# Kernel tuning notes

Measured on AMD Instinct MI355X. Metric: run time of the kernel, lower is better.

## Reference

```python
import jax, jax.numpy as jnp
import numpy as np

N_NODES = 100000
N_EDGES = 3200000
N_GRAPHS = 1000
C = 11   # atomic features
D = 4    # bond features
BN_EPS = 1e-5


def setup_inputs() -> dict:
    key = jax.random.key(0)
    ks = jax.random.split(key, 20)
    inp = {
        "x": jax.random.normal(ks[0], (N_NODES, C), dtype=jnp.float32),
        "edge_index": jax.random.randint(ks[1], (2, N_EDGES), 0, N_NODES),
        "edge_attr": jax.random.uniform(ks[2], (N_EDGES, D), dtype=jnp.float32),
        "batch": jnp.sort(jax.random.randint(ks[3], (N_NODES,), 0, N_GRAPHS)),
    }
    s = 0.3
    # CGConv layer 1 params: lin_f, lin_s take z=[x_i, x_j, e] of dim 2C+D
    inp["Wf1"] = jax.random.normal(ks[4], (2 * C + D, C), dtype=jnp.float32) * s
    inp["bf1"] = jnp.zeros((C,), jnp.float32)
    inp["Ws1"] = jax.random.normal(ks[5], (2 * C + D, C), dtype=jnp.float32) * s
    inp["bs1"] = jnp.zeros((C,), jnp.float32)
    inp["gamma1"] = jnp.ones((C,), jnp.float32)
    inp["beta1"] = jnp.zeros((C,), jnp.float32)
    # CGConv layer 2
    inp["Wf2"] = jax.random.normal(ks[6], (2 * C + D, C), dtype=jnp.float32) * s
    inp["bf2"] = jnp.zeros((C,), jnp.float32)
    inp["Ws2"] = jax.random.normal(ks[7], (2 * C + D, C), dtype=jnp.float32) * s
    inp["bs2"] = jnp.zeros((C,), jnp.float32)
    inp["gamma2"] = jnp.ones((C,), jnp.float32)
    inp["beta2"] = jnp.zeros((C,), jnp.float32)
    # MLP head
    inp["W_fc1"] = jax.random.normal(ks[8], (C, 5), dtype=jnp.float32) * s
    inp["b_fc1"] = jnp.zeros((5,), jnp.float32)
    inp["W_fc2"] = jax.random.normal(ks[9], (5, 1), dtype=jnp.float32) * s
    inp["b_fc2"] = jnp.zeros((1,), jnp.float32)
    return inp


def _cgconv(x, src, dst, e, Wf, bf, Ws, bs, gamma, beta):
    # z = [x_i, x_j, e_ij] per edge; message = sigmoid(lin_f(z)) * softplus(lin_s(z))
    z = jnp.concatenate([x[dst], x[src], e], axis=-1)          # [E, 2C+D]
    msg = jax.nn.sigmoid(z @ Wf + bf) * jax.nn.softplus(z @ Ws + bs)  # [E, C]
    agg = jax.ops.segment_sum(msg, dst, num_segments=N_NODES)  # [N, C]
    # BatchNorm1d (training-mode: batch statistics over nodes)
    mu = jnp.mean(agg, axis=0)
    var = jnp.var(agg, axis=0)
    agg = (agg - mu) * jax.lax.rsqrt(var + BN_EPS) * gamma + beta
    return x + agg  # residual


def reference(x, edge_index, edge_attr, batch,
              Wf1, bf1, Ws1, bs1, gamma1, beta1,
              Wf2, bf2, Ws2, bs2, gamma2, beta2,
              W_fc1, b_fc1, W_fc2, b_fc2):
    src, dst = edge_index[0], edge_index[1]
    h = _cgconv(x, src, dst, edge_attr, Wf1, bf1, Ws1, bs1, gamma1, beta1)
    h = _cgconv(h, src, dst, edge_attr, Wf2, bf2, Ws2, bs2, gamma2, beta2)
    # global mean pool per graph
    sums = jax.ops.segment_sum(h, batch, num_segments=N_GRAPHS)        # [G, C]
    cnts = jax.ops.segment_sum(jnp.ones((h.shape[0],), h.dtype), batch,
                               num_segments=N_GRAPHS)
    pooled = sums / jnp.maximum(cnts, 1.0)[:, None]
    out = jax.nn.softplus(pooled @ W_fc1 + b_fc1)
    out = out @ W_fc2 + b_fc2                                          # [G, 1]
    return out
```

## Files before the change

kernel.cpp:

```cpp
#include <hip/hip_runtime.h>
#include <hip/hip_fp16.h>
#include <math.h>

#define N_NODES 100000
#define N_EDGES 3200000
#define N_GRAPHS 1000
#define C 11
#define D 4
#define AST 12
#define XWST 24
#define XHST 16
#define BN_EPS 1e-5f
#define LOG2E 1.44269504088896f
#define LN2   0.69314718055994f
#define QSCALE (1.0f/65535.0f)

#define BSHIFT 8
#define BNODES 256
#define NB ((N_NODES + BNODES - 1) / BNODES)
#define SUBS 8
#define CAP2 1280
#define EPB 8192
#define PBLK ((N_EDGES + EPB - 1) / EPB)
#define SB 64
#define PST 48

__device__ __forceinline__ float fast_sigmoid(float x) {
    float e = exp2f(-LOG2E * x);
    return __builtin_amdgcn_rcpf(1.0f + e);
}
__device__ __forceinline__ float fast_softplus(float x) {
    float e = exp2f(LOG2E * x);
    float l = log2f(1.0f + e) * LN2;
    return (x > 20.0f) ? x : l;
}
__device__ __forceinline__ unsigned packh2(float a, float b) {
    __half2 h = __floats2half2_rn(a, b);
    return *reinterpret_cast<unsigned*>(&h);
}
__device__ __forceinline__ float2 unpackh2(unsigned u) {
    __half2 h = *reinterpret_cast<__half2*>(&u);
    return __half22float2(h);
}

__global__ void __launch_bounds__(1024) partition_kernel(
    const int* __restrict__ ei, const float4* __restrict__ ea,
    int* __restrict__ bcur2, uint3* __restrict__ grp)
{
    __shared__ int lh[NB];
    __shared__ int lbase[NB];
    for (int i = threadIdx.x; i < NB; i += 1024) lh[i] = 0;
    __syncthreads();
    int sub = blockIdx.x & (SUBS - 1);
    int e0 = blockIdx.x * EPB;
    for (int r = 0; r < EPB; r += 1024) {
        int e = e0 + r + threadIdx.x;
        if (e < N_EDGES) atomicAdd(&lh[ei[N_EDGES + e] >> BSHIFT], 1);
    }
    __syncthreads();
    for (int b = threadIdx.x; b < NB; b += 1024) {
        lbase[b] = atomicAdd(&bcur2[b * SUBS + sub], lh[b]);
        lh[b] = 0;
    }
    __syncthreads();
    for (int r = 0; r < EPB; r += 1024) {
        int e = e0 + r + threadIdx.x;
        if (e < N_EDGES) {
            int d = ei[N_EDGES + e];
            int s = ei[e];
            float4 v = ea[e];
            unsigned q0 = (unsigned)(v.x * 65535.0f + 0.5f);
            unsigned q1 = (unsigned)(v.y * 65535.0f + 0.5f);
            unsigned q2 = (unsigned)(v.z * 65535.0f + 0.5f);
            unsigned q3 = (unsigned)(v.w * 65535.0f + 0.5f);
            int b = d >> BSHIFT;
            int ofs = lbase[b] + atomicAdd(&lh[b], 1);
            if (ofs < CAP2)
                grp[((size_t)b * SUBS + sub) * CAP2 + ofs] =
                    make_uint3((unsigned)s | ((unsigned)(d & 255) << 17),
                               q0 | (q1 << 16), q2 | (q3 << 16));
        }
    }
}

__global__ void __launch_bounds__(512) bscan_kernel(
    const int* __restrict__ bcur2, int* __restrict__ bexcl, int* __restrict__ off)
{
    __shared__ int wsum[8];
    int t = threadIdx.x;
    int lane = t & 63, w = t >> 6;
    int v = 0;
    if (t < NB) {
        #pragma unroll
        for (int s = 0; s < SUBS; ++s) v += min(bcur2[t * SUBS + s], CAP2);
    }
    int incl = v;
    #pragma unroll
    for (int d = 1; d < 64; d <<= 1) {
        int u = __shfl_up(incl, d);
        if (lane >= d) incl += u;
    }
    if (lane == 63) wsum[w] = incl;
    __syncthreads();
    if (w == 0) {
        int x = (lane < 8) ? wsum[lane] : 0;
        #pragma unroll
        for (int d = 1; d < 8; d <<= 1) {
            int u = __shfl_up(x, d);
            if (lane >= d) x += u;
        }
        if (lane < 8) wsum[lane] = x;
    }
    __syncthreads();
    int excl = incl - v + (w > 0 ? wsum[w - 1] : 0);
    if (t < NB) bexcl[t] = excl;
    if (t == NB - 1) off[N_NODES] = excl + v;
}

__global__ void __launch_bounds__(512) finalize_kernel(
    const uint3* __restrict__ grp, const int* __restrict__ bcur2,
    const int* __restrict__ bexcl,
    int* __restrict__ off, uint3* __restrict__ rec)
{
    __shared__ int lcnt[BNODES];
    __shared__ int lexcl[BNODES];
    __shared__ int wsum[4];
    int b = blockIdx.x;
    int base = bexcl[b];
    int t = threadIdx.x;
    if (t < BNODES) lcnt[t] = 0;
    __syncthreads();
    for (int s = 0; s < SUBS; ++s) {
        int cs = min(bcur2[b * SUBS + s], CAP2);
        const uint3* g = grp + ((size_t)b * SUBS + s) * CAP2;
        for (int i = t; i < cs; i += 512)
            atomicAdd(&lcnt[(g[i].x >> 17) & 255], 1);
    }
    __syncthreads();
    if (t < BNODES) {
        int lane = t & 63, w = t >> 6;
        int v = lcnt[t];
        int incl = v;
        #pragma unroll
        for (int d = 1; d < 64; d <<= 1) {
            int u = __shfl_up(incl, d);
            if (lane >= d) incl += u;
        }
        if (lane == 63) wsum[w] = incl;
        __syncthreads();
        if (w == 0) {
            int x = (lane < 4) ? wsum[lane] : 0;
            #pragma unroll
            for (int d = 1; d < 4; d <<= 1) {
                int u = __shfl_up(x, d);
                if (lane >= d) x += u;
            }
            if (lane < 4) wsum[lane] = x;
        }
        __syncthreads();
        int excl = incl - v + (w > 0 ? wsum[w - 1] : 0);
        lexcl[t] = excl;
        int n = (b << BSHIFT) + t;
        if (n < N_NODES) off[n] = base + excl;
        lcnt[t] = 0;
    } else {
        __syncthreads();
        __syncthreads();
    }
    __syncthreads();
    for (int s = 0; s < SUBS; ++s) {
        int cs = min(bcur2[b * SUBS + s], CAP2);
        const uint3* g = grp + ((size_t)b * SUBS + s) * CAP2;
        for (int i = t; i < cs; i += 512) {
            uint3 r = g[i];
            int nl = (r.x >> 17) & 255;
            int pos = base + lexcl[nl] + atomicAdd(&lcnt[nl], 1);
            rec[pos] = make_uint3(r.x & 0x1FFFFu, r.y, r.z);
        }
    }
}

__global__ void __launch_bounds__(256) pre_kernel(
    const float* __restrict__ xin, int stride,
    const float* __restrict__ Wf, const float* __restrict__ Ws,
    const float* __restrict__ bf, const float* __restrict__ bs,
    float* __restrict__ xwd, unsigned* __restrict__ xwsh)
{
    __shared__ float sW[22 * C * 2];
    __shared__ float sbf[C], sbs[C];
    for (int i = threadIdx.x; i < 22 * C; i += blockDim.x) {
        sW[2 * i] = Wf[i];
        sW[2 * i + 1] = Ws[i];
    }
    if (threadIdx.x < C) { sbf[threadIdx.x] = bf[threadIdx.x]; sbs[threadIdx.x] = bs[threadIdx.x]; }
    __syncthreads();

    int n = blockIdx.x * blockDim.x + threadIdx.x;
    if (n >= N_NODES) return;
    float xi[C];
    #pragma unroll
    for (int j = 0; j < C; ++j) xi[j] = xin[n * stride + j];

    float od[XWST];
    unsigned oh[12];
    #pragma unroll
    for (int c = 0; c < C; ++c) {
        float f = sbf[c], s = sbs[c];
        float f2 = 0.0f, s2 = 0.0f;
        #pragma unroll
        for (int j = 0; j < C; ++j) {
            f  = fmaf(xi[j], sW[2 * (j * C + c)], f);
            s  = fmaf(xi[j], sW[2 * (j * C + c) + 1], s);
            f2 = fmaf(xi[j], sW[2 * ((C + j) * C + c)], f2);
            s2 = fmaf(xi[j], sW[2 * ((C + j) * C + c) + 1], s2);
        }
        od[2 * c] = f; od[2 * c + 1] = s;
        oh[c] = packh2(f2, s2);
    }
    od[22] = 0.0f; od[23] = 0.0f; oh[11] = 0u;
    float4* pd = (float4*)(xwd + (size_t)n * XWST);
    #pragma unroll
    for (int i = 0; i < 6; ++i)
        pd[i] = make_float4(od[4 * i], od[4 * i + 1], od[4 * i + 2], od[4 * i + 3]);
    uint4* ph = (uint4*)(xwsh + (size_t)n * XHST);
    #pragma unroll
    for (int i = 0; i < 3; ++i)
        ph[i] = make_uint4(oh[4 * i], oh[4 * i + 1], oh[4 * i + 2], oh[4 * i + 3]);
}

__global__ void __launch_bounds__(256) conv_kernel(
    const uint3* __restrict__ rec, const int* __restrict__ off,
    const float* __restrict__ xwd, const unsigned* __restrict__ xwsh,
    const float* __restrict__ Wf, const float* __restrict__ Ws,
    float* __restrict__ agg)
{
    int tid = blockIdx.x * blockDim.x + threadIdx.x;
    int n = tid >> 3;
    int t = tid & 7;
    if (n >= N_NODES) return;

    float weaf[44], weas[44];
    {
        const float2* pf = (const float2*)(Wf + 22 * C);
        const float2* ps = (const float2*)(Ws + 22 * C);
        #pragma unroll
        for (int i = 0; i < 22; ++i) {
            float2 a = pf[i], b = ps[i];
            weaf[2 * i] = a.x; weaf[2 * i + 1] = a.y;
            weas[2 * i] = b.x; weas[2 * i + 1] = b.y;
        }
    }
    float based[XWST];
    {
        const float4* pd = (const float4*)(xwd + (size_t)n * XWST);
        #pragma unroll
        for (int i = 0; i < 6; ++i) {
            float4 a = pd[i];
            based[4 * i] = a.x; based[4 * i + 1] = a.y;
            based[4 * i + 2] = a.z; based[4 * i + 3] = a.w;
        }
    }

    float acc[C];
    #pragma unroll
    for (int c = 0; c < C; ++c) acc[c] = 0.0f;

    int e1 = off[n + 1];
    for (int k = off[n] + t; k < e1; k += 8) {
        uint3 r = rec[k];
        int src = (int)r.x;
        float ea0 = (float)(r.y & 0xFFFFu) * QSCALE;
        float ea1 = (float)(r.y >> 16) * QSCALE;
        float ea2 = (float)(r.z & 0xFFFFu) * QSCALE;
        float ea3 = (float)(r.z >> 16) * QSCALE;
        const uint4* px = (const uint4*)(xwsh + (size_t)src * XHST);
        uint4 ha = px[0], hb = px[1], hc = px[2];
        float2 xv[C];
        xv[0] = unpackh2(ha.x); xv[1] = unpackh2(ha.y);
        xv[2] = unpackh2(ha.z); xv[3] = unpackh2(ha.w);
        xv[4] = unpackh2(hb.x); xv[5] = unpackh2(hb.y);
        xv[6] = unpackh2(hb.z); xv[7] = unpackh2(hb.w);
        xv[8] = unpackh2(hc.x); xv[9] = unpackh2(hc.y);
        xv[10] = unpackh2(hc.z);
        #pragma unroll
        for (int c = 0; c < C; ++c) {
            float f = based[2 * c] + xv[c].x;
            float s = based[2 * c + 1] + xv[c].y;
            f = fmaf(ea0, weaf[c], f);         s = fmaf(ea0, weas[c], s);
            f = fmaf(ea1, weaf[C + c], f);     s = fmaf(ea1, weas[C + c], s);
            f = fmaf(ea2, weaf[2 * C + c], f); s = fmaf(ea2, weas[2 * C + c], s);
            f = fmaf(ea3, weaf[3 * C + c], f); s = fmaf(ea3, weas[3 * C + c], s);
            acc[c] += fast_sigmoid(f) * fast_softplus(s);
        }
    }

    #pragma unroll
    for (int c = 0; c < C; ++c) {
        acc[c] += __shfl_xor(acc[c], 1);
        acc[c] += __shfl_xor(acc[c], 2);
        acc[c] += __shfl_xor(acc[c], 4);
    }
    if (t == 0) {
        float4* pa = (float4*)(agg + (size_t)n * AST);
        pa[0] = make_float4(acc[0], acc[1], acc[2], acc[3]);
        pa[1] = make_float4(acc[4], acc[5], acc[6], acc[7]);
        pa[2] = make_float4(acc[8], acc[9], acc[10], 0.0f);
    }
}

__global__ void __launch_bounds__(256) bn_stats_kernel(
    const float* __restrict__ agg, float* __restrict__ pstats)
{
    float s[C], q[C];
    #pragma unroll
    for (int c = 0; c < C; ++c) { s[c] = 0.0f; q[c] = 0.0f; }
    for (int n = blockIdx.x * 256 + threadIdx.x; n < N_NODES; n += SB * 256) {
        const float4* pa = (const float4*)(agg + (size_t)n * AST);
        float4 a0 = pa[0], a1 = pa[1], a2 = pa[2];
        float v[C] = {a0.x, a0.y, a0.z, a0.w, a1.x, a1.y, a1.z, a1.w,
                      a2.x, a2.y, a2.z};
        #pragma unroll
        for (int c = 0; c < C; ++c) { s[c] += v[c]; q[c] += v[c] * v[c]; }
    }
    #pragma unroll
    for (int c = 0; c < C; ++c) {
        #pragma unroll
        for (int o = 32; o > 0; o >>= 1) {
            s[c] += __shfl_down(s[c], o);
            q[c] += __shfl_down(q[c], o);
        }
    }
    __shared__ float ls[2 * C + 2];
    if (threadIdx.x < 2 * C + 2) ls[threadIdx.x] = 0.0f;
    __syncthreads();
    if ((threadIdx.x & 63) == 0) {
        #pragma unroll
        for (int c = 0; c < C; ++c) {
            atomicAdd(&ls[2 * c], s[c]);
            atomicAdd(&ls[2 * c + 1], q[c]);
        }
    }
    __syncthreads();
    if (threadIdx.x < 2 * C)
        pstats[blockIdx.x * PST + threadIdx.x] = ls[threadIdx.x];
}

__device__ __forceinline__ void reduce_stats(
    const float* __restrict__ pstats, float* smu, float* srs)
{
    if (threadIdx.x < C) {
        double sum = 0.0, sq = 0.0;
        for (int b = 0; b < SB; ++b) {
            sum += (double)pstats[b * PST + 2 * threadIdx.x];
            sq  += (double)pstats[b * PST + 2 * threadIdx.x + 1];
        }
        double mu = sum / (double)N_NODES;
        double var = sq / (double)N_NODES - mu * mu;
        smu[threadIdx.x] = (float)mu;
        srs[threadIdx.x] = (float)(1.0 / sqrt(var + (double)BN_EPS));
    }
}

__global__ void __launch_bounds__(256) bnpre_kernel(
    const float* __restrict__ xin, const float* __restrict__ agg,
    const float* __restrict__ pstats,
    const float* __restrict__ gamma, const float* __restrict__ beta,
    const float* __restrict__ Wf, const float* __restrict__ Ws,
    const float* __restrict__ bf, const float* __restrict__ bs,
    float* __restrict__ hout, float* __restrict__ xwd, unsigned* __restrict__ xwsh)
{
    __shared__ float sW[22 * C * 2];
    __shared__ float sbf[C], sbs[C];
    __shared__ float smu[C], srs[C], sg[C], sb[C];
    for (int i = threadIdx.x; i < 22 * C; i += blockDim.x) {
        sW[2 * i] = Wf[i];
        sW[2 * i + 1] = Ws[i];
    }
    reduce_stats(pstats, smu, srs);
    if (threadIdx.x < C) {
        sbf[threadIdx.x] = bf[threadIdx.x];
        sbs[threadIdx.x] = bs[threadIdx.x];
        sg[threadIdx.x] = gamma[threadIdx.x];
        sb[threadIdx.x] = beta[threadIdx.x];
    }
    __syncthreads();

    int n = blockIdx.x * blockDim.x + threadIdx.x;
    if (n >= N_NODES) return;

    float hv[C];
    #pragma unroll
    for (int c = 0; c < C; ++c) {
        float a = agg[n * AST + c];
        hv[c] = xin[n * C + c] + (a - smu[c]) * srs[c] * sg[c] + sb[c];
    }
    {
        float4* ph = (float4*)(hout + (size_t)n * AST);
        ph[0] = make_float4(hv[0], hv[1], hv[2], hv[3]);
        ph[1] = make_float4(hv[4], hv[5], hv[6], hv[7]);
        ph[2] = make_float4(hv[8], hv[9], hv[10], 0.0f);
    }

    float od[XWST];
    unsigned oh[12];
    #pragma unroll
    for (int c = 0; c < C; ++c) {
        float f = sbf[c], s = sbs[c];
        float f2 = 0.0f, s2 = 0.0f;
        #pragma unroll
        for (int j = 0; j < C; ++j) {
            f  = fmaf(hv[j], sW[2 * (j * C + c)], f);
            s  = fmaf(hv[j], sW[2 * (j * C + c) + 1], s);
            f2 = fmaf(hv[j], sW[2 * ((C + j) * C + c)], f2);
            s2 = fmaf(hv[j], sW[2 * ((C + j) * C + c) + 1], s2);
        }
        od[2 * c] = f; od[2 * c + 1] = s;
        oh[c] = packh2(f2, s2);
    }
    od[22] = 0.0f; od[23] = 0.0f; oh[11] = 0u;
    float4* pd = (float4*)(xwd + (size_t)n * XWST);
    #pragma unroll
    for (int i = 0; i < 6; ++i)
        pd[i] = make_float4(od[4 * i], od[4 * i + 1], od[4 * i + 2], od[4 * i + 3]);
    uint4* ph2 = (uint4*)(xwsh + (size_t)n * XHST);
    #pragma unroll
    for (int i = 0; i < 3; ++i)
        ph2[i] = make_uint4(oh[4 * i], oh[4 * i + 1], oh[4 * i + 2], oh[4 * i + 3]);
}

__global__ void __launch_bounds__(256) bn_apply_kernel(
    const float* __restrict__ hin, const float* __restrict__ agg,
    const float* __restrict__ pstats,
    const float* __restrict__ gamma, const float* __restrict__ beta,
    float* __restrict__ hout)
{
    __shared__ float smu[C], srs[C], sg[C], sb[C];
    reduce_stats(pstats, smu, srs);
    if (threadIdx.x < C) {
        sg[threadIdx.x] = gamma[threadIdx.x];
        sb[threadIdx.x] = beta[threadIdx.x];
    }
    __syncthreads();
    int n = blockIdx.x * blockDim.x + threadIdx.x;
    if (n >= N_NODES) return;
    float hv[C];
    #pragma unroll
    for (int c = 0; c < C; ++c) {
        float a = agg[n * AST + c];
        hv[c] = hin[n * AST + c] + (a - smu[c]) * srs[c] * sg[c] + sb[c];
    }
    float4* ph = (float4*)(hout + (size_t)n * AST);
    ph[0] = make_float4(hv[0], hv[1], hv[2], hv[3]);
    ph[1] = make_float4(hv[4], hv[5], hv[6], hv[7]);
    ph[2] = make_float4(hv[8], hv[9], hv[10], 0.0f);
}

__global__ void __launch_bounds__(256) pool_kernel(
    const float* __restrict__ h, const int* __restrict__ batch,
    float* __restrict__ gsum, float* __restrict__ gcnt)
{
    const int PER = 8;
    int t = blockIdx.x * blockDim.x + threadIdx.x;
    int start = t * PER;
    if (start >= N_NODES) return;
    int end = min(start + PER, N_NODES);

    int g = batch[start];
    float acc[C];
    #pragma unroll
    for (int c = 0; c < C; ++c) acc[c] = 0.0f;
    float cnt = 0.0f;
    for (int n = start; n < end; ++n) {
        int gn = batch[n];
        if (gn != g) {
            #pragma unroll
            for (int c = 0; c < C; ++c) atomicAdd(&gsum[g * C + c], acc[c]);
            atomicAdd(&gcnt[g], cnt);
            g = gn;
            #pragma unroll
            for (int c = 0; c < C; ++c) acc[c] = 0.0f;
            cnt = 0.0f;
        }
        #pragma unroll
        for (int c = 0; c < C; ++c) acc[c] += h[n * AST + c];
        cnt += 1.0f;
    }
    #pragma unroll
    for (int c = 0; c < C; ++c) atomicAdd(&gsum[g * C + c], acc[c]);
    atomicAdd(&gcnt[g], cnt);
}

__global__ void __launch_bounds__(256) head_kernel(
    const float* __restrict__ gsum, const float* __restrict__ gcnt,
    const float* __restrict__ W1, const float* __restrict__ b1,
    const float* __restrict__ W2, const float* __restrict__ b2,
    float* __restrict__ out)
{
    int g = blockIdx.x * blockDim.x + threadIdx.x;
    if (g >= N_GRAPHS) return;
    float cnt = fmaxf(gcnt[g], 1.0f);
    float p[C];
    #pragma unroll
    for (int c = 0; c < C; ++c) p[c] = gsum[g * C + c] / cnt;
    float acc = b2[0];
    #pragma unroll
    for (int j = 0; j < 5; ++j) {
        float t = b1[j];
        #pragma unroll
        for (int c = 0; c < C; ++c) t = fmaf(p[c], W1[c * 5 + j], t);
        acc = fmaf(fast_softplus(t), W2[j], acc);
    }
    out[g] = acc;
}

extern "C" void kernel_launch(void* const* d_in, const int* in_sizes, int n_in,
                              void* d_out, int out_size, void* d_ws, size_t ws_size,
                              hipStream_t stream) {
    const float* x   = (const float*)d_in[0];
    const int*   ei  = (const int*)d_in[1];
    const float* ea  = (const float*)d_in[2];
    const int*   bat = (const int*)d_in[3];
    const float* Wf1 = (const float*)d_in[4];
    const float* bf1 = (const float*)d_in[5];
    const float* Ws1 = (const float*)d_in[6];
    const float* bs1 = (const float*)d_in[7];
    const float* g1  = (const float*)d_in[8];
    const float* be1 = (const float*)d_in[9];
    const float* Wf2 = (const float*)d_in[10];
    const float* bf2 = (const float*)d_in[11];
    const float* Ws2 = (const float*)d_in[12];
    const float* bs2 = (const float*)d_in[13];
    const float* g2  = (const float*)d_in[14];
    const float* be2 = (const float*)d_in[15];
    const float* W_fc1 = (const float*)d_in[16];
    const float* b_fc1 = (const float*)d_in[17];
    const float* W_fc2 = (const float*)d_in[18];
    const float* b_fc2 = (const float*)d_in[19];
    float* out = (float*)d_out;

    char* ws = (char*)d_ws;
    size_t o = 0;
    size_t zz0 = o;
    int*      bcur2 = (int*)(ws + o);      o += (size_t)NB * SUBS * 4;
    float*    gsum  = (float*)(ws + o);    o += (size_t)N_GRAPHS * C * 4;
    float*    gcnt  = (float*)(ws + o);    o += (size_t)N_GRAPHS * 4;
    size_t zsize = o - zz0;
    int*      bexcl = (int*)(ws + o);      o += (size_t)(NB + 1) * 4;
    int*      off   = (int*)(ws + o);      o += (size_t)(N_NODES + 1) * 4;
    o = (o + 255) & ~(size_t)255;
    float*    pst1  = (float*)(ws + o);    o += (size_t)SB * PST * 4;
    float*    pst2  = (float*)(ws + o);    o += (size_t)SB * PST * 4;
    o = (o + 255) & ~(size_t)255;
    uint3*    grp   = (uint3*)(ws + o);    o += (size_t)NB * SUBS * CAP2 * 12;
    o = (o + 255) & ~(size_t)255;
    uint3*    rec   = (uint3*)(ws + o);    o += (size_t)N_EDGES * 12;
    o = (o + 255) & ~(size_t)255;
    float*    xwd   = (float*)(ws + o);    o += (size_t)N_NODES * XWST * 4;
    o = (o + 255) & ~(size_t)255;
    unsigned* xwsh  = (unsigned*)(ws + o); o += (size_t)N_NODES * XHST * 4;
    float*    agg   = (float*)(ws + o);    o += (size_t)N_NODES * AST * 4;
    float*    h1    = (float*)(ws + o);    o += (size_t)N_NODES * AST * 4;
    float*    h2    = xwd;

    const int cblocks = (N_NODES * 8 + 255) / 256;
    const int nblocks = (N_NODES + 255) / 256;

    hipMemsetAsync(ws + zz0, 0, zsize, stream);

    partition_kernel<<<PBLK, 1024, 0, stream>>>(ei, (const float4*)ea, bcur2, grp);
    bscan_kernel<<<1, 512, 0, stream>>>(bcur2, bexcl, off);
    finalize_kernel<<<NB, 512, 0, stream>>>(grp, bcur2, bexcl, off, rec);

    pre_kernel<<<nblocks, 256, 0, stream>>>(x, C, Wf1, Ws1, bf1, bs1, xwd, xwsh);
    conv_kernel<<<cblocks, 256, 0, stream>>>(rec, off, xwd, xwsh, Wf1, Ws1, agg);
    bn_stats_kernel<<<SB, 256, 0, stream>>>(agg, pst1);
    bnpre_kernel<<<nblocks, 256, 0, stream>>>(x, agg, pst1, g1, be1,
                                              Wf2, Ws2, bf2, bs2, h1, xwd, xwsh);

    conv_kernel<<<cblocks, 256, 0, stream>>>(rec, off, xwd, xwsh, Wf2, Ws2, agg);
    bn_stats_kernel<<<SB, 256, 0, stream>>>(agg, pst2);
    bn_apply_kernel<<<nblocks, 256, 0, stream>>>(h1, agg, pst2, g2, be2, h2);

    pool_kernel<<<(N_NODES / 8 + 255) / 256, 256, 0, stream>>>(h2, bat, gsum, gcnt);
    head_kernel<<<(N_GRAPHS + 255) / 256, 256, 0, stream>>>(gsum, gcnt, W_fc1, b_fc1,
                                                            W_fc2, b_fc2, out);
}
```

Baseline: 310.1 us.

## Stage partitioned edge records in shared memory for coalesced bucket writes

The partition kernel now processes edges in chunks of 4096. Each chunk is counting-sorted by destination bucket into LDS and then written to the global bucket arrays in bucket order, so consecutive threads write contiguous addresses instead of scattering 12-byte records. This adds extra LDS histograms, a single-wave prefix scan, and several more block barriers per chunk, and raises shared-memory use (about 60KB), which may reduce occupancy.

```diff
diff --git a/kernel.cpp b/kernel.cpp
--- a/kernel.cpp
+++ b/kernel.cpp
@@ -21,6 +21,7 @@
 #define SUBS 8
 #define CAP2 1280
 #define EPB 8192
+#define CHUNK 4096
 #define PBLK ((N_EDGES + EPB - 1) / EPB)
 #define SB 64
 #define PST 48
@@ -49,37 +50,82 @@
 {
     __shared__ int lh[NB];
     __shared__ int lbase[NB];
-    for (int i = threadIdx.x; i < NB; i += 1024) lh[i] = 0;
-    __syncthreads();
+    __shared__ int lwr[NB];
+    __shared__ int ccnt[NB];
+    __shared__ uint3 srec[CHUNK];
+    __shared__ unsigned short sbk[CHUNK];
+
+    int t = threadIdx.x;
     int sub = blockIdx.x & (SUBS - 1);
     int e0 = blockIdx.x * EPB;
+
+    for (int i = t; i < NB; i += 1024) { lh[i] = 0; lwr[i] = 0; }
+    __syncthreads();
     for (int r = 0; r < EPB; r += 1024) {
-        int e = e0 + r + threadIdx.x;
+        int e = e0 + r + t;
         if (e < N_EDGES) atomicAdd(&lh[ei[N_EDGES + e] >> BSHIFT], 1);
     }
     __syncthreads();
-    for (int b = threadIdx.x; b < NB; b += 1024) {
+    for (int b = t; b < NB; b += 1024)
         lbase[b] = atomicAdd(&bcur2[b * SUBS + sub], lh[b]);
-        lh[b] = 0;
-    }
-    __syncthreads();
-    for (int r = 0; r < EPB; r += 1024) {
-        int e = e0 + r + threadIdx.x;
-        if (e < N_EDGES) {
-            int d = ei[N_EDGES + e];
-            int s = ei[e];
-            float4 v = ea[e];
-            unsigned q0 = (unsigned)(v.x * 65535.0f + 0.5f);
-            unsigned q1 = (unsigned)(v.y * 65535.0f + 0.5f);
-            unsigned q2 = (unsigned)(v.z * 65535.0f + 0.5f);
-            unsigned q3 = (unsigned)(v.w * 65535.0f + 0.5f);
-            int b = d >> BSHIFT;
-            int ofs = lbase[b] + atomicAdd(&lh[b], 1);
-            if (ofs < CAP2)
-                grp[((size_t)b * SUBS + sub) * CAP2 + ofs] =
-                    make_uint3((unsigned)s | ((unsigned)(d & 255) << 17),
-                               q0 | (q1 << 16), q2 | (q3 << 16));
-        }
+    __syncthreads();
+
+    for (int cbase = 0; cbase < EPB; cbase += CHUNK) {
+        int nrec = N_EDGES - (e0 + cbase);
+        nrec = nrec < 0 ? 0 : (nrec > CHUNK ? CHUNK : nrec);
+        if (nrec == 0) break;
+
+        for (int i = t; i < NB; i += 1024) ccnt[i] = 0;
+        __syncthreads();
+        for (int r = 0; r < CHUNK; r += 1024) {
+            int e = e0 + cbase + r + t;
+            if (e < N_EDGES)
+                atomicAdd(&ccnt[ei[N_EDGES + e] >> BSHIFT], 1);
+        }
+        __syncthreads();
+        if (t < 64) {
+            int lo = t * 7, hi = min(lo + 7, NB);
+            int s = 0;
+            for (int i = lo; i < hi; ++i) s += ccnt[i];
+            int v = s;
+            #pragma unroll
+            for (int d = 1; d < 64; d <<= 1) {
+                int u = __shfl_up(v, d);
+                if (t >= d) v += u;
+            }
+            int run = v - s;
+            for (int i = lo; i < hi; ++i) { lh[i] = run; run += ccnt[i]; }
+        }
+        __syncthreads();
+        for (int i = t; i < NB; i += 1024) ccnt[i] = 0;
+        __syncthreads();
+        for (int r = 0; r < CHUNK; r += 1024) {
+            int e = e0 + cbase + r + t;
+            if (e < N_EDGES) {
+                int d = ei[N_EDGES + e];
+                int s = ei[e];
+                float4 v = ea[e];
+                unsigned q0 = (unsigned)(v.x * 65535.0f + 0.5f);
+                unsigned q1 = (unsigned)(v.y * 65535.0f + 0.5f);
+                unsigned q2 = (unsigned)(v.z * 65535.0f + 0.5f);
+                unsigned q3 = (unsigned)(v.w * 65535.0f + 0.5f);
+                int b = d >> BSHIFT;
+                int k = lh[b] + atomicAdd(&ccnt[b], 1);
+                srec[k] = make_uint3((unsigned)s | ((unsigned)(d & 255) << 17),
+                                     q0 | (q1 << 16), q2 | (q3 << 16));
+                sbk[k] = (unsigned short)b;
+            }
+        }
+        __syncthreads();
+        for (int k = t; k < nrec; k += 1024) {
+            int b = sbk[k];
+            int o2 = lbase[b] + lwr[b] + (k - lh[b]);
+            if (o2 < CAP2)
+                grp[((size_t)b * SUBS + sub) * CAP2 + o2] = srec[k];
+        }
+        __syncthreads();
+        for (int b = t; b < NB; b += 1024) lwr[b] += ccnt[b];
+        __syncthreads();
     }
 }
 
```

New measurement: 299.1 us. 3.5% less time.
